# Performance work log

Hardware: AMD Instinct MI355X
Metric: run time of the kernel (lower is better)

## Reference

```python
import jax, jax.numpy as jnp
import numpy as np

B, S, D = 2, 2048, 1024
H, DH = 16, 64          # n_heads, size_per_head; H*DH == D
FF = 4096               # hidden_dim
EPS = 1e-6              # flax LayerNorm default


def _layernorm(x, scale, bias):
    mu = jnp.mean(x, axis=-1, keepdims=True)
    var = jnp.mean(jnp.square(x - mu), axis=-1, keepdims=True)
    return (x - mu) * jax.lax.rsqrt(var + EPS) * scale + bias


def setup_inputs() -> dict:
    key = jax.random.key(0)
    ks = jax.random.split(key, 12)
    p = lambda k, shape: (jax.random.normal(k, shape, dtype=jnp.float32) * 0.02)
    return {
        "X": jax.random.normal(ks[0], (B, S, D), dtype=jnp.float32),
        "mask": jax.random.randint(ks[1], (B, S), 0, 2, dtype=jnp.int32),
        "Wq": p(ks[2], (D, H * DH)), "bq": jnp.zeros((H * DH,), jnp.float32),
        "Wk": p(ks[3], (D, H * DH)), "bk": jnp.zeros((H * DH,), jnp.float32),
        "Wv": p(ks[4], (D, H * DH)), "bv": jnp.zeros((H * DH,), jnp.float32),
        "Wo": p(ks[5], (H * DH, D)), "bo": jnp.zeros((D,), jnp.float32),
        "ln0_scale": jnp.ones((D,), jnp.float32), "ln0_bias": jnp.zeros((D,), jnp.float32),
        "W1": p(ks[6], (D, FF)), "b1": jnp.zeros((FF,), jnp.float32),
        "W2": p(ks[7], (FF, D)), "b2": jnp.zeros((D,), jnp.float32),
        "ln1_scale": jnp.ones((D,), jnp.float32), "ln1_bias": jnp.zeros((D,), jnp.float32),
    }


def reference(X, mask, Wq, bq, Wk, bk, Wv, bv, Wo, bo,
              ln0_scale, ln0_bias, W1, b1, W2, b2, ln1_scale, ln1_bias):
    b, n, d = X.shape

    def proj(x, W, bias):
        # (B,S,D) -> (B,H,S,DH)
        return (x @ W + bias).reshape(b, n, H, DH).swapaxes(1, 2)

    q = proj(X, Wq, bq)
    k = proj(X, Wk, bk)
    v = proj(X, Wv, bv)

    # scaled dot-product attention with additive padding mask
    scores = jnp.einsum('bhnd,bhmd->bhnm', q, k) / jnp.sqrt(jnp.asarray(DH, X.dtype))
    m = mask[:, None, None, :].astype(scores.dtype)  # (B,1,1,M)
    scores = scores + m * -10000.0
    attn = jax.nn.softmax(scores, axis=-1)
    out = jnp.einsum('bhnm,bhmd->bhnd', attn, v)      # (B,H,S,DH)
    out = out.swapaxes(1, 2).reshape(b, n, H * DH)
    out = out @ Wo + bo

    # add & norm
    X1 = _layernorm(X + out, ln0_scale, ln0_bias)

    # feed-forward
    ff = jnp.maximum(X1 @ W1 + b1, 0.0) @ W2 + b2

    # add & norm
    return _layernorm(X1 + ff, ln1_scale, ln1_bias)
```

## Files before the change

### kernel.cpp

```cpp
#include <hip/hip_runtime.h>
#include <hip/hip_bf16.h>
#include <stdint.h>

#define B_ 2
#define S_ 2048
#define D_ 1024
#define H_ 16
#define DH_ 64
#define FF_ 4096
#define M_ (B_*S_)

typedef __bf16 bf16;
typedef __bf16 bf16x4 __attribute__((ext_vector_type(4)));
typedef __bf16 bf16x8 __attribute__((ext_vector_type(8)));
typedef float f32x4 __attribute__((ext_vector_type(4)));

#define LOG2E 1.44269504f

__device__ __forceinline__ float fexp2(float x) {
#if __has_builtin(__builtin_amdgcn_exp2f)
  return __builtin_amdgcn_exp2f(x);
#else
  return exp2f(x);
#endif
}

__device__ __forceinline__ void gload_lds16(const void* g, void* l) {
  auto gp = reinterpret_cast<const __attribute__((address_space(1))) void*>(
      reinterpret_cast<uintptr_t>(g));
  auto lp = reinterpret_cast<__attribute__((address_space(3))) void*>(
      reinterpret_cast<uintptr_t>(l));
  __builtin_amdgcn_global_load_lds(gp, lp, 16, 0, 0);
}

__global__ __launch_bounds__(256) void prep_all(
    const float* __restrict__ X, bf16* __restrict__ Xb,
    const float* __restrict__ bq, const float* __restrict__ bk,
    const float* __restrict__ bv, float* __restrict__ bqkv,
    const int* __restrict__ mask, float* __restrict__ Mp,
    const float* __restrict__ Wq, const float* __restrict__ Wk,
    const float* __restrict__ Wv, const float* __restrict__ Wo,
    const float* __restrict__ W1, const float* __restrict__ W2,
    bf16* __restrict__ Wqkvt, bf16* __restrict__ Wot,
    bf16* __restrict__ W1t, bf16* __restrict__ W2t) {
  int bid = blockIdx.x;
  const int tid = threadIdx.x;
  if (bid < 4096) {
    int i = (bid * 256 + tid) * 4;
    float4 v = *(const float4*)(X + i);
    Xb[i+0] = (bf16)v.x; Xb[i+1] = (bf16)v.y;
    Xb[i+2] = (bf16)v.z; Xb[i+3] = (bf16)v.w;
    return;
  }
  bid -= 4096;
  if (bid < 12) {
    int i = bid * 256 + tid;
    bqkv[i] = i < 1024 ? bq[i] : (i < 2048 ? bk[i-1024] : bv[i-2048]);
    return;
  }
  bid -= 12;
  if (bid < 16) {
    int i = bid * 256 + tid;
    Mp[i] = (-10000.0f * LOG2E) * (float)mask[i];
    return;
  }
  bid -= 16;
  const float* src; bf16* dst; int K, N;
  if (bid < 1024)      { src = Wq; dst = Wqkvt;                     K=1024; N=1024; }
  else if (bid < 2048) { src = Wk; dst = Wqkvt + (size_t)1024*1024; K=1024; N=1024; bid -= 1024; }
  else if (bid < 3072) { src = Wv; dst = Wqkvt + (size_t)2048*1024; K=1024; N=1024; bid -= 2048; }
  else if (bid < 4096) { src = Wo; dst = Wot;                       K=1024; N=1024; bid -= 3072; }
  else if (bid < 8192) { src = W1; dst = W1t;                       K=1024; N=4096; bid -= 4096; }
  else                 { src = W2; dst = W2t;                       K=4096; N=1024; bid -= 8192; }
  __shared__ float t[32][33];
  const int tx = tid & 31, ty = tid >> 5;
  const int nt32 = N >> 5;
  const int n0 = (bid % nt32) * 32, k0 = (bid / nt32) * 32;
#pragma unroll
  for (int i = 0; i < 4; i++)
    t[ty + i*8][tx] = src[(size_t)(k0 + ty + i*8) * N + n0 + tx];
  __syncthreads();
#pragma unroll
  for (int i = 0; i < 4; i++)
    dst[(size_t)(n0 + ty + i*8) * K + k0 + tx] = (bf16)t[tx][ty + i*8];
}
#define PREP_BLOCKS (4096 + 12 + 16 + 4*1024 + 2*4096)

__global__ __launch_bounds__(256) void transpose_v(
    const bf16* __restrict__ QKV, bf16* __restrict__ Vt) {
  __shared__ bf16 t[64][66];
  int bh = blockIdx.x, s0 = blockIdx.y * 64;
  int b = bh >> 4, h = bh & 15;
  int w = threadIdx.x >> 6, l = threadIdx.x & 63;
#pragma unroll
  for (int i = 0; i < 16; i++) {
    int sr = w*16 + i;
    t[sr][l] = QKV[(size_t)(b*S_ + s0 + sr) * 3072 + 2*D_ + h*DH_ + l];
  }
  __syncthreads();
  const int pcol = (l & 15) * 4 + (l >> 4);
#pragma unroll
  for (int i = 0; i < 16; i++) {
    int dh = w*16 + i;
    Vt[((size_t)(bh*DH_ + dh)) * S_ + s0 + pcol] = t[l][dh];
  }
}

template<int SK>
__global__ __launch_bounds__(256) void gemm_sk(
    const bf16* __restrict__ A, const bf16* __restrict__ Bt,
    const float* __restrict__ bias, float* __restrict__ Cp,
    int M, int N, int K) {
  __shared__ bf16 As[2][128*32];
  __shared__ bf16 Bs[2][128*32];
  const int tid = threadIdx.x;
  const int w = tid >> 6, l = tid & 63;
  const int wm = w >> 1, wn = w & 1;
  const int r16 = l & 15, g = l >> 4;

  const int gx = gridDim.x, gxy = gx * gridDim.y;
  const int nwg = gxy * SK;
  const int lid = (blockIdx.z * gridDim.y + blockIdx.y) * gx + blockIdx.x;
  const int swz = (lid & 7) * (nwg >> 3) + (lid >> 3);
  const int z = swz / gxy, rem = swz % gxy;
  const int m0 = (rem / gx) * 128, n0 = (rem % gx) * 128;
  const int kc = K / SK, kb = z * kc;

  const int srow = w*16 + (l >> 2);
  const int acol8 = (l & 3) * 8;
  const bf16* ag = A + (size_t)(m0 + srow) * K + acol8;
  const bf16* bg = Bt + (size_t)(n0 + srow) * K + acol8;

  f32x4 acc[4][4];
#pragma unroll
  for (int i = 0; i < 4; i++)
#pragma unroll
    for (int j = 0; j < 4; j++) acc[i][j] = (f32x4){0.f,0.f,0.f,0.f};

#pragma unroll
  for (int p = 0; p < 2; p++) {
    gload_lds16(ag + (size_t)(p*64) * K + kb, &As[0][(p*64 + w*16) * 32]);
    gload_lds16(bg + (size_t)(p*64) * K + kb, &Bs[0][(p*64 + w*16) * 32]);
  }
  asm volatile("s_waitcnt vmcnt(0)" ::: "memory");
  __builtin_amdgcn_s_barrier();
  asm volatile("" ::: "memory");

  const int nt = kc >> 5;
  int cur = 0;
  for (int t = 0; t < nt; ++t) {
    if (t + 1 < nt) {
      const int k0 = kb + (t + 1) * 32;
#pragma unroll
      for (int p = 0; p < 2; p++) {
        gload_lds16(ag + (size_t)(p*64) * K + k0, &As[cur^1][(p*64 + w*16) * 32]);
        gload_lds16(bg + (size_t)(p*64) * K + k0, &Bs[cur^1][(p*64 + w*16) * 32]);
      }
    }
    bf16x8 af[4], bfr[4];
#pragma unroll
    for (int mi = 0; mi < 4; mi++)
      af[mi] = *(const bf16x8*)&As[cur][(wm*64 + mi*16 + r16) * 32 + g*8];
#pragma unroll
    for (int ni = 0; ni < 4; ni++)
      bfr[ni] = *(const bf16x8*)&Bs[cur][(wn*64 + ni*16 + r16) * 32 + g*8];
    __builtin_amdgcn_s_setprio(1);
#pragma unroll
    for (int mi = 0; mi < 4; mi++)
#pragma unroll
      for (int ni = 0; ni < 4; ni++)
        acc[mi][ni] = __builtin_amdgcn_mfma_f32_16x16x32_bf16(
            af[mi], bfr[ni], acc[mi][ni], 0, 0, 0);
    __builtin_amdgcn_s_setprio(0);

    asm volatile("s_waitcnt vmcnt(0)" ::: "memory");
    __builtin_amdgcn_s_barrier();
    asm volatile("" ::: "memory");
    cur ^= 1;
  }

  float* outp = Cp + (size_t)z * M * N;
  float bvs[4];
#pragma unroll
  for (int ni = 0; ni < 4; ni++)
    bvs[ni] = (z == 0) ? bias[n0 + wn*64 + ni*16 + r16] : 0.f;
#pragma unroll
  for (int mi = 0; mi < 4; mi++)
#pragma unroll
    for (int ni = 0; ni < 4; ni++)
#pragma unroll
      for (int r = 0; r < 4; r++) {
        size_t row = (size_t)(m0 + wm*64 + mi*16 + g*4 + r);
        size_t col = (size_t)(n0 + wn*64 + ni*16 + r16);
        outp[row * N + col] = acc[mi][ni][r] + bvs[ni];
      }
}

template<bool RELU>
__global__ __launch_bounds__(512) void gemm256(
    const bf16* __restrict__ A, const bf16* __restrict__ Bt,
    const float* __restrict__ bias, bf16* __restrict__ C,
    int M, int N, int K) {
  __shared__ bf16 As[2][256*64];
  __shared__ bf16 Bs[2][256*64];
  const int tid = threadIdx.x;
  const int w = tid >> 6, l = tid & 63;
  const int wm = w >> 2, wn = w & 3;
  const int r16 = l & 15, g = l >> 4;

  const int gx = gridDim.x;
  const int nwg = gx * gridDim.y;
  const int lid = blockIdx.y * gx + blockIdx.x;
  const int swz = (lid & 7) * (nwg >> 3) + (lid >> 3);
  const int m0 = (swz / gx) * 256, n0 = (swz % gx) * 256;

  const int srow = w*8 + (l >> 3);
  const int sch  = ((l & 7) ^ (l >> 3)) * 8;
  const bf16* ag = A  + (size_t)(m0 + srow) * K + sch;
  const bf16* bg = Bt + (size_t)(n0 + srow) * K + sch;

  f32x4 acc[8][4];
#pragma unroll
  for (int i = 0; i < 8; i++)
#pragma unroll
    for (int j = 0; j < 4; j++) acc[i][j] = (f32x4){0.f,0.f,0.f,0.f};

#pragma unroll
  for (int q = 0; q < 4; q++) {
    gload_lds16(ag + (size_t)(q*64) * K, &As[0][(q*64 + w*8) * 64]);
    gload_lds16(bg + (size_t)(q*64) * K, &Bs[0][(q*64 + w*8) * 64]);
  }
  asm volatile("s_waitcnt vmcnt(0)" ::: "memory");
  __builtin_amdgcn_s_barrier();
  asm volatile("" ::: "memory");

  const int nt = K >> 6;
  int cur = 0;
  for (int t = 0; t < nt; ++t) {
    if (t + 1 < nt) {
      const size_t k0 = (size_t)(t + 1) << 6;
#pragma unroll
      for (int q = 0; q < 4; q++) {
        gload_lds16(ag + (size_t)(q*64) * K + k0, &As[cur^1][(q*64 + w*8) * 64]);
        gload_lds16(bg + (size_t)(q*64) * K + k0, &Bs[cur^1][(q*64 + w*8) * 64]);
      }
    }

    bf16x8 af[4][2], blo[2][2], bhi[2][2];
#pragma unroll
    for (int mi = 0; mi < 4; mi++)
#pragma unroll
      for (int kk = 0; kk < 2; kk++) {
        const int row = wm*128 + mi*16 + r16;
        af[mi][kk] = *(const bf16x8*)&As[cur][row*64 + (((kk*4+g) ^ (row & 7)))*8];
      }
#pragma unroll
    for (int ni = 0; ni < 2; ni++)
#pragma unroll
      for (int kk = 0; kk < 2; kk++) {
        const int row = wn*64 + ni*16 + r16;
        blo[ni][kk] = *(const bf16x8*)&Bs[cur][row*64 + (((kk*4+g) ^ (row & 7)))*8];
      }
    __builtin_amdgcn_s_setprio(1);
#pragma unroll
    for (int mi = 0; mi < 4; mi++)
#pragma unroll
      for (int ni = 0; ni < 2; ni++)
#pragma unroll
        for (int kk = 0; kk < 2; kk++)
          acc[mi][ni] = __builtin_amdgcn_mfma_f32_16x16x32_bf16(
              af[mi][kk], blo[ni][kk], acc[mi][ni], 0, 0, 0);
    __builtin_amdgcn_s_setprio(0);
#pragma unroll
    for (int ni = 0; ni < 2; ni++)
#pragma unroll
      for (int kk = 0; kk < 2; kk++) {
        const int row = wn*64 + 32 + ni*16 + r16;
        bhi[ni][kk] = *(const bf16x8*)&Bs[cur][row*64 + (((kk*4+g) ^ (row & 7)))*8];
      }
    __builtin_amdgcn_s_setprio(1);
#pragma unroll
    for (int mi = 0; mi < 4; mi++)
#pragma unroll
      for (int ni = 0; ni < 2; ni++)
#pragma unroll
        for (int kk = 0; kk < 2; kk++)
          acc[mi][2+ni] = __builtin_amdgcn_mfma_f32_16x16x32_bf16(
              af[mi][kk], bhi[ni][kk], acc[mi][2+ni], 0, 0, 0);
    __builtin_amdgcn_s_setprio(0);
#pragma unroll
    for (int mi = 0; mi < 4; mi++)
#pragma unroll
      for (int kk = 0; kk < 2; kk++) {
        const int row = wm*128 + 64 + mi*16 + r16;
        af[mi][kk] = *(const bf16x8*)&As[cur][row*64 + (((kk*4+g) ^ (row & 7)))*8];
      }
    __builtin_amdgcn_s_setprio(1);
#pragma unroll
    for (int mi = 0; mi < 4; mi++)
#pragma unroll
      for (int ni = 0; ni < 2; ni++)
#pragma unroll
        for (int kk = 0; kk < 2; kk++)
          acc[4+mi][2+ni] = __builtin_amdgcn_mfma_f32_16x16x32_bf16(
              af[mi][kk], bhi[ni][kk], acc[4+mi][2+ni], 0, 0, 0);
    __builtin_amdgcn_s_setprio(0);
    __builtin_amdgcn_s_setprio(1);
#pragma unroll
    for (int mi = 0; mi < 4; mi++)
#pragma unroll
      for (int ni = 0; ni < 2; ni++)
#pragma unroll
        for (int kk = 0; kk < 2; kk++)
          acc[4+mi][ni] = __builtin_amdgcn_mfma_f32_16x16x32_bf16(
              af[mi][kk], blo[ni][kk], acc[4+mi][ni], 0, 0, 0);
    __builtin_amdgcn_s_setprio(0);

    asm volatile("s_waitcnt vmcnt(0)" ::: "memory");
    __builtin_amdgcn_s_barrier();
    asm volatile("" ::: "memory");
    cur ^= 1;
  }

  float bvs[4];
#pragma unroll
  for (int ni = 0; ni < 4; ni++) bvs[ni] = bias[n0 + wn*64 + ni*16 + r16];
#pragma unroll
  for (int mi = 0; mi < 8; mi++)
#pragma unroll
    for (int ni = 0; ni < 4; ni++)
#pragma unroll
      for (int r = 0; r < 4; r++) {
        float v = acc[mi][ni][r] + bvs[ni];
        if (RELU) v = fmaxf(v, 0.f);
        C[(size_t)(m0 + wm*128 + mi*16 + g*4 + r) * N +
          (n0 + wn*64 + ni*16 + r16)] = (bf16)v;
      }
}

__global__ __launch_bounds__(256) void attn(
    const bf16* __restrict__ QKV, const bf16* __restrict__ Vt,
    const float* __restrict__ Mp, bf16* __restrict__ AO) {
  __shared__ bf16 Ks[2][64*64];
  __shared__ bf16 Vs[2][64*64];
  __shared__ bf16 Ps[4][32*72];

  const float SC2 = 0.125f * LOG2E;
  const int bh = blockIdx.x, b = bh >> 4, h = bh & 15;
  const int q0 = blockIdx.y * 128;
  const int tid = threadIdx.x, w = tid >> 6, l = tid & 63;
  const int r16 = l & 15, g = l >> 4;
  const int qw = q0 + w*32;

  bf16x8 qf[2][2];
#pragma unroll
  for (int s = 0; s < 2; s++)
#pragma unroll
    for (int kk = 0; kk < 2; kk++)
      qf[s][kk] = *(const bf16x8*)&QKV[((size_t)(b*S_ + qw + s*16 + r16))*3072
                                       + h*64 + kk*32 + g*8];

  const int srow = w*8 + (l >> 3);
  const int sch  = (l & 7) ^ (l >> 3);
  const bf16* kg = QKV + ((size_t)(b*S_) + srow)*3072 + 1024 + h*64 + sch*8;
  const bf16* vg = Vt + ((size_t)(bh*64 + srow))*S_ + sch*8;

  f32x4 po[2][4];
#pragma unroll
  for (int s = 0; s < 2; s++)
#pragma unroll
    for (int n = 0; n < 4; n++) po[s][n] = (f32x4){0.f,0.f,0.f,0.f};
  float mrun[8], lsum[8];
#pragma unroll
  for (int r = 0; r < 8; r++) { mrun[r] = -1.0e30f; lsum[r] = 0.f; }

  float madd[4];
#pragma unroll
  for (int ct = 0; ct < 4; ct++) madd[ct] = Mp[b*S_ + ct*16 + r16];
#pragma unroll
  for (int p = 0; p < 2; p++) {
    gload_lds16(kg + (size_t)(p*32)*3072, &Ks[0][(p*256 + w*64)*8]);
    gload_lds16(vg + (size_t)(p*32)*S_,   &Vs[0][(p*256 + w*64)*8]);
  }

  const int NT = S_/64;
  int cur = 0;
  for (int it = 0; it < NT; ++it) {
    const int kv0 = it * 64;
    if (it + 1 < NT) {
#pragma unroll
      for (int p = 0; p < 2; p++) {
        gload_lds16(kg + (size_t)(kv0 + 64 + p*32)*3072, &Ks[cur^1][(p*256 + w*64)*8]);
        gload_lds16(vg + (size_t)(p*32)*S_ + (kv0 + 64), &Vs[cur^1][(p*256 + w*64)*8]);
      }
      asm volatile("s_waitcnt vmcnt(4)" ::: "memory");
    } else {
      asm volatile("s_waitcnt vmcnt(0)" ::: "memory");
    }
    __builtin_amdgcn_s_barrier();
    asm volatile("" ::: "memory");

    float sv[2][4][4];
    __builtin_amdgcn_s_setprio(1);
#pragma unroll
    for (int ct = 0; ct < 4; ct++) {
      const int row = ct*16 + r16;
      bf16x8 kf0 = *(const bf16x8*)&Ks[cur][row*64 + ((g) ^ (row & 7))*8];
      bf16x8 kf1 = *(const bf16x8*)&Ks[cur][row*64 + ((4+g) ^ (row & 7))*8];
      f32x4 a0 = (f32x4){0.f,0.f,0.f,0.f}, a1 = (f32x4){0.f,0.f,0.f,0.f};
      a0 = __builtin_amdgcn_mfma_f32_16x16x32_bf16(qf[0][0], kf0, a0, 0, 0, 0);
      a0 = __builtin_amdgcn_mfma_f32_16x16x32_bf16(qf[0][1], kf1, a0, 0, 0, 0);
      a1 = __builtin_amdgcn_mfma_f32_16x16x32_bf16(qf[1][0], kf0, a1, 0, 0, 0);
      a1 = __builtin_amdgcn_mfma_f32_16x16x32_bf16(qf[1][1], kf1, a1, 0, 0, 0);
#pragma unroll
      for (int r = 0; r < 4; r++) {
        sv[0][ct][r] = a0[r]*SC2 + madd[ct];
        sv[1][ct][r] = a1[r]*SC2 + madd[ct];
      }
    }
    __builtin_amdgcn_s_setprio(0);

    if (it + 1 < NT) {
#pragma unroll
      for (int ct = 0; ct < 4; ct++)
        madd[ct] = Mp[b*S_ + kv0 + 64 + ct*16 + r16];
    }

    float lmax[8];
#pragma unroll
    for (int s = 0; s < 2; s++)
#pragma unroll
      for (int r = 0; r < 4; r++)
        lmax[s*4+r] = fmaxf(fmaxf(sv[s][0][r], sv[s][1][r]),
                            fmaxf(sv[s][2][r], sv[s][3][r]));
    bool grow = false;
#pragma unroll
    for (int i = 0; i < 8; i++) grow |= (lmax[i] > mrun[i] + 8.f);
    if (__any(grow)) {
#pragma unroll
      for (int s = 0; s < 2; s++)
#pragma unroll
        for (int r = 0; r < 4; r++) {
          const int i = s*4 + r;
          float t = lmax[i];
#pragma unroll
          for (int off = 8; off >= 1; off >>= 1) t = fmaxf(t, __shfl_xor(t, off, 16));
          float mnew = fmaxf(mrun[i], t);
          float sc = fexp2(mrun[i] - mnew);
          mrun[i] = mnew;
          lsum[i] *= sc;
#pragma unroll
          for (int n = 0; n < 4; n++) po[s][n][r] *= sc;
        }
    }
#pragma unroll
    for (int s = 0; s < 2; s++)
#pragma unroll
      for (int r = 0; r < 4; r++) {
        const int i = s*4 + r;
#pragma unroll
        for (int ct = 0; ct < 4; ct++)
          sv[s][ct][r] = fexp2(sv[s][ct][r] - mrun[i]);
        lsum[i] += (sv[s][0][r] + sv[s][1][r]) + (sv[s][2][r] + sv[s][3][r]);
      }

#pragma unroll
    for (int s = 0; s < 2; s++)
#pragma unroll
      for (int r = 0; r < 4; r++) {
        bf16x4 pk;
#pragma unroll
        for (int ct = 0; ct < 4; ct++) pk[ct] = (bf16)sv[s][ct][r];
        *(bf16x4*)&Ps[w][(s*16 + g*4 + r)*72 + r16*4] = pk;
      }
    asm volatile("s_waitcnt lgkmcnt(0)" ::: "memory");

    __builtin_amdgcn_s_setprio(1);
#pragma unroll
    for (int kk = 0; kk < 2; kk++) {
      bf16x8 pa0 = *(const bf16x8*)&Ps[w][(r16)*72 + kk*32 + g*8];
      bf16x8 pa1 = *(const bf16x8*)&Ps[w][(16 + r16)*72 + kk*32 + g*8];
#pragma unroll
      for (int n = 0; n < 4; n++) {
        const int row = n*16 + r16;
        bf16x8 vf = *(const bf16x8*)&Vs[cur][row*64 + ((kk*4 + g) ^ (row & 7))*8];
        po[0][n] = __builtin_amdgcn_mfma_f32_16x16x32_bf16(pa0, vf, po[0][n], 0, 0, 0);
        po[1][n] = __builtin_amdgcn_mfma_f32_16x16x32_bf16(pa1, vf, po[1][n], 0, 0, 0);
      }
    }
    __builtin_amdgcn_s_setprio(0);

    __builtin_amdgcn_s_barrier();
    asm volatile("" ::: "memory");
    cur ^= 1;
  }

#pragma unroll
  for (int i = 0; i < 8; i++) {
    float t = lsum[i];
#pragma unroll
    for (int off = 8; off >= 1; off >>= 1) t += __shfl_xor(t, off, 16);
    lsum[i] = t;
  }

#pragma unroll
  for (int s = 0; s < 2; s++)
#pragma unroll
    for (int n = 0; n < 4; n++)
#pragma unroll
      for (int r = 0; r < 4; r++) {
        float v = po[s][n][r] / lsum[s*4 + r];
        AO[(size_t)(b*S_ + qw + s*16 + g*4 + r)*D_ + h*64 + n*16 + r16] = (bf16)v;
      }
}

template<bool XF32, bool OUTF32>
__global__ __launch_bounds__(256) void ln_res2(
    const void* __restrict__ xp, const float* __restrict__ p0,
    const float* __restrict__ p1, const float* __restrict__ sc,
    const float* __restrict__ bi, float* __restrict__ y,
    bf16* __restrict__ yb) {
  const int row = blockIdx.x, tid = threadIdx.x;
  const size_t base = (size_t)row * D_;
  float xv[4];
  if (XF32) {
    float4 a = ((const float4*)((const float*)xp + base))[tid];
    xv[0] = a.x; xv[1] = a.y; xv[2] = a.z; xv[3] = a.w;
  } else {
    bf16x4 a = ((const bf16x4*)((const bf16*)xp + base))[tid];
#pragma unroll
    for (int j = 0; j < 4; j++) xv[j] = (float)a[j];
  }
  float4 a0 = ((const float4*)(p0 + base))[tid];
  float4 a1 = ((const float4*)(p1 + base))[tid];
  float v[4] = {xv[0] + a0.x + a1.x, xv[1] + a0.y + a1.y,
                xv[2] + a0.z + a1.z, xv[3] + a0.w + a1.w};
  float s  = v[0] + v[1] + v[2] + v[3];
  float ss = v[0]*v[0] + v[1]*v[1] + v[2]*v[2] + v[3]*v[3];
#pragma unroll
  for (int off = 32; off >= 1; off >>= 1) {
    s  += __shfl_xor(s, off, 64);
    ss += __shfl_xor(ss, off, 64);
  }
  __shared__ float red[8];
  const int wv = tid >> 6;
  if ((tid & 63) == 0) { red[wv] = s; red[4 + wv] = ss; }
  __syncthreads();
  s  = red[0] + red[1] + red[2] + red[3];
  ss = red[4] + red[5] + red[6] + red[7];
  const float mu  = s * (1.0f / D_);
  const float inv = rsqrtf(ss * (1.0f / D_) - mu*mu + 1e-6f);
  float4 scv = ((const float4*)sc)[tid];
  float4 biv = ((const float4*)bi)[tid];
  float o[4];
  o[0] = (v[0]-mu)*inv*scv.x + biv.x;
  o[1] = (v[1]-mu)*inv*scv.y + biv.y;
  o[2] = (v[2]-mu)*inv*scv.z + biv.z;
  o[3] = (v[3]-mu)*inv*scv.w + biv.w;
  if (OUTF32) {
    ((float4*)(y + base))[tid] = make_float4(o[0], o[1], o[2], o[3]);
  } else {
    bf16x4 ob;
#pragma unroll
    for (int j = 0; j < 4; j++) ob[j] = (bf16)o[j];
    *(bf16x4*)&yb[base + tid*4] = ob;
  }
}

extern "C" void kernel_launch(void* const* d_in, const int* in_sizes, int n_in,
                              void* d_out, int out_size, void* d_ws, size_t ws_size,
                              hipStream_t stream) {
  const float* X    = (const float*)d_in[0];
  const int*   mask = (const int*)d_in[1];
  const float* Wq   = (const float*)d_in[2];
  const float* bq   = (const float*)d_in[3];
  const float* Wk   = (const float*)d_in[4];
  const float* bk   = (const float*)d_in[5];
  const float* Wv   = (const float*)d_in[6];
  const float* bv   = (const float*)d_in[7];
  const float* Wo   = (const float*)d_in[8];
  const float* bo   = (const float*)d_in[9];
  const float* ln0s = (const float*)d_in[10];
  const float* ln0b = (const float*)d_in[11];
  const float* W1   = (const float*)d_in[12];
  const float* b1   = (const float*)d_in[13];
  const float* W2   = (const float*)d_in[14];
  const float* b2   = (const float*)d_in[15];
  const float* ln1s = (const float*)d_in[16];
  const float* ln1b = (const float*)d_in[17];
  float* out = (float*)d_out;

  char* ws = (char*)d_ws;
  const size_t MB = 1024 * 1024;
  bf16*  Xb    = (bf16*)(ws + 0);
  bf16*  AO    = (bf16*)(ws + 0);
  bf16*  X1b   = (bf16*)(ws + 0);
  bf16*  Wqkvt = (bf16*)(ws + 8*MB);
  bf16*  Wot   = (bf16*)(ws + 14*MB);
  bf16*  W1t   = (bf16*)(ws + 16*MB);
  bf16*  W2t   = (bf16*)(ws + 24*MB);
  bf16*  QKV   = (bf16*)(ws + 32*MB);
  bf16*  Vt    = (bf16*)(ws + 56*MB);
  bf16*  FF1   = (bf16*)(ws + 32*MB);
  float* P0    = (float*)(ws + 64*MB);
  float* P1    = (float*)(ws + 80*MB);
  float* bqkv  = (float*)(ws + 64*MB);
  float* Mp    = (float*)(ws + 64*MB + 16384);

  prep_all<<<PREP_BLOCKS, 256, 0, stream>>>(
      X, Xb, bq, bk, bv, bqkv, mask, Mp,
      Wq, Wk, Wv, Wo, W1, W2, Wqkvt, Wot, W1t, W2t);

  gemm256<false><<<dim3(3072/256, M_/256), 512, 0, stream>>>(Xb, Wqkvt, bqkv, QKV, M_, 3072, D_);
  transpose_v<<<dim3(32, S_/64), 256, 0, stream>>>(QKV, Vt);
  attn<<<dim3(32, S_/128), 256, 0, stream>>>(QKV, Vt, Mp, AO);
  gemm_sk<2><<<dim3(D_/128, M_/128, 2), 256, 0, stream>>>(AO, Wot, bo, P0, M_, D_, D_);
  ln_res2<true,false><<<M_, 256, 0, stream>>>(X, P0, P1, ln0s, ln0b, nullptr, X1b);
  gemm256<true><<<dim3(FF_/256, M_/256), 512, 0, stream>>>(X1b, W1t, b1, FF1, M_, FF_, D_);
  gemm_sk<2><<<dim3(D_/128, M_/128, 2), 256, 0, stream>>>(FF1, W2t, b2, P0, M_, D_, FF_);
  ln_res2<false,true><<<M_, 256, 0, stream>>>(X1b, P0, P1, ln1s, ln1b, out, nullptr);
}
```

Measured before the change: 228.0 us.

## Split attention over two KV halves with a combine kernel

The attention kernel now splits the key/value sequence into two halves along a new grid dimension, doubling the block count from 512 to 1024. Each half writes unnormalized bf16 partial outputs plus per-row max and sum, and a new attn_combine kernel merges them with log-sum-exp rescaling. The P tile in shared memory shrinks to one 16-row subtile processed per s iteration with swizzled addressing, and launch bounds request 4 blocks per CU to raise occupancy. In exchange it adds an extra launch, extra global traffic for the partials, and bf16 rounding of unnormalized partial outputs.

```diff
diff --git a/kernel.cpp b/kernel.cpp
--- a/kernel.cpp
+++ b/kernel.cpp
@@ -338,16 +338,19 @@
       }
 }
 
-__global__ __launch_bounds__(256) void attn(
+__global__ __launch_bounds__(256, 4) void attn(
     const bf16* __restrict__ QKV, const bf16* __restrict__ Vt,
-    const float* __restrict__ Mp, bf16* __restrict__ AO) {
+    const float* __restrict__ Mp, bf16* __restrict__ Op,
+    float2* __restrict__ ML) {
   __shared__ bf16 Ks[2][64*64];
   __shared__ bf16 Vs[2][64*64];
-  __shared__ bf16 Ps[4][32*72];
+  __shared__ bf16 Ps[4][16*64];
 
   const float SC2 = 0.125f * LOG2E;
   const int bh = blockIdx.x, b = bh >> 4, h = bh & 15;
   const int q0 = blockIdx.y * 128;
+  const int z  = blockIdx.z;
+  const int kvb = z * (S_/2);
   const int tid = threadIdx.x, w = tid >> 6, l = tid & 63;
   const int r16 = l & 15, g = l >> 4;
   const int qw = q0 + w*32;
@@ -362,8 +365,8 @@
 
   const int srow = w*8 + (l >> 3);
   const int sch  = (l & 7) ^ (l >> 3);
-  const bf16* kg = QKV + ((size_t)(b*S_) + srow)*3072 + 1024 + h*64 + sch*8;
-  const bf16* vg = Vt + ((size_t)(bh*64 + srow))*S_ + sch*8;
+  const bf16* kg = QKV + ((size_t)(b*S_) + kvb + srow)*3072 + 1024 + h*64 + sch*8;
+  const bf16* vg = Vt + ((size_t)(bh*64 + srow))*S_ + kvb + sch*8;
 
   f32x4 po[2][4];
 #pragma unroll
@@ -376,14 +379,14 @@
 
   float madd[4];
 #pragma unroll
-  for (int ct = 0; ct < 4; ct++) madd[ct] = Mp[b*S_ + ct*16 + r16];
+  for (int ct = 0; ct < 4; ct++) madd[ct] = Mp[b*S_ + kvb + ct*16 + r16];
 #pragma unroll
   for (int p = 0; p < 2; p++) {
     gload_lds16(kg + (size_t)(p*32)*3072, &Ks[0][(p*256 + w*64)*8]);
     gload_lds16(vg + (size_t)(p*32)*S_,   &Vs[0][(p*256 + w*64)*8]);
   }
 
-  const int NT = S_/64;
+  const int NT = (S_/2)/64;
   int cur = 0;
   for (int it = 0; it < NT; ++it) {
     const int kv0 = it * 64;
@@ -423,7 +426,7 @@
     if (it + 1 < NT) {
 #pragma unroll
       for (int ct = 0; ct < 4; ct++)
-        madd[ct] = Mp[b*S_ + kv0 + 64 + ct*16 + r16];
+        madd[ct] = Mp[b*S_ + kvb + kv0 + 64 + ct*16 + r16];
     }
 
     float lmax[8];
@@ -465,30 +468,30 @@
       }
 
 #pragma unroll
-    for (int s = 0; s < 2; s++)
+    for (int s = 0; s < 2; s++) {
 #pragma unroll
       for (int r = 0; r < 4; r++) {
         bf16x4 pk;
 #pragma unroll
         for (int ct = 0; ct < 4; ct++) pk[ct] = (bf16)sv[s][ct][r];
-        *(bf16x4*)&Ps[w][(s*16 + g*4 + r)*72 + r16*4] = pk;
-      }
-    asm volatile("s_waitcnt lgkmcnt(0)" ::: "memory");
-
-    __builtin_amdgcn_s_setprio(1);
-#pragma unroll
-    for (int kk = 0; kk < 2; kk++) {
-      bf16x8 pa0 = *(const bf16x8*)&Ps[w][(r16)*72 + kk*32 + g*8];
-      bf16x8 pa1 = *(const bf16x8*)&Ps[w][(16 + r16)*72 + kk*32 + g*8];
-#pragma unroll
-      for (int n = 0; n < 4; n++) {
-        const int row = n*16 + r16;
-        bf16x8 vf = *(const bf16x8*)&Vs[cur][row*64 + ((kk*4 + g) ^ (row & 7))*8];
-        po[0][n] = __builtin_amdgcn_mfma_f32_16x16x32_bf16(pa0, vf, po[0][n], 0, 0, 0);
-        po[1][n] = __builtin_amdgcn_mfma_f32_16x16x32_bf16(pa1, vf, po[1][n], 0, 0, 0);
-      }
+        const int row = g*4 + r;
+        const int c = (r16 >> 1) ^ (row & 7);
+        *(bf16x4*)&Ps[w][row*64 + c*8 + (r16 & 1)*4] = pk;
+      }
+      asm volatile("s_waitcnt lgkmcnt(0)" ::: "memory");
+      __builtin_amdgcn_s_setprio(1);
+#pragma unroll
+      for (int kk = 0; kk < 2; kk++) {
+        bf16x8 pa = *(const bf16x8*)&Ps[w][r16*64 + (((kk*4+g) ^ (r16 & 7)))*8];
+#pragma unroll
+        for (int n = 0; n < 4; n++) {
+          const int row = n*16 + r16;
+          bf16x8 vf = *(const bf16x8*)&Vs[cur][row*64 + ((kk*4 + g) ^ (row & 7))*8];
+          po[s][n] = __builtin_amdgcn_mfma_f32_16x16x32_bf16(pa, vf, po[s][n], 0, 0, 0);
+        }
+      }
+      __builtin_amdgcn_s_setprio(0);
     }
-    __builtin_amdgcn_s_setprio(0);
 
     __builtin_amdgcn_s_barrier();
     asm volatile("" ::: "memory");
@@ -508,10 +511,40 @@
 #pragma unroll
     for (int n = 0; n < 4; n++)
 #pragma unroll
-      for (int r = 0; r < 4; r++) {
-        float v = po[s][n][r] / lsum[s*4 + r];
-        AO[(size_t)(b*S_ + qw + s*16 + g*4 + r)*D_ + h*64 + n*16 + r16] = (bf16)v;
-      }
+      for (int r = 0; r < 4; r++)
+        Op[(size_t)z*M_*D_ + (size_t)(b*S_ + qw + s*16 + g*4 + r)*D_
+           + h*64 + n*16 + r16] = (bf16)po[s][n][r];
+  if (r16 == 0) {
+#pragma unroll
+    for (int s = 0; s < 2; s++)
+#pragma unroll
+      for (int r = 0; r < 4; r++)
+        ML[((size_t)z*32 + bh)*S_ + qw + s*16 + g*4 + r] =
+            make_float2(mrun[s*4 + r], lsum[s*4 + r]);
+  }
+}
+
+__global__ __launch_bounds__(256) void attn_combine(
+    const bf16* __restrict__ Op, const float2* __restrict__ ML,
+    bf16* __restrict__ AO) {
+  const int t = blockIdx.x;
+  const int tid = threadIdx.x;
+  const int d0 = tid * 4;
+  const int h = d0 >> 6;
+  const int q = t & (S_ - 1), b = t >> 11;
+  const int bh = b*16 + h;
+  float2 ml0 = ML[(size_t)bh*S_ + q];
+  float2 ml1 = ML[((size_t)32 + bh)*S_ + q];
+  float m = fmaxf(ml0.x, ml1.x);
+  float a0 = fexp2(ml0.x - m), a1 = fexp2(ml1.x - m);
+  float inv = 1.0f / (ml0.y*a0 + ml1.y*a1);
+  bf16x4 o0 = *(const bf16x4*)&Op[(size_t)t*D_ + d0];
+  bf16x4 o1 = *(const bf16x4*)&Op[(size_t)M_*D_ + (size_t)t*D_ + d0];
+  bf16x4 o;
+#pragma unroll
+  for (int j = 0; j < 4; j++)
+    o[j] = (bf16)(((float)o0[j]*a0 + (float)o1[j]*a1) * inv);
+  *(bf16x4*)&AO[(size_t)t*D_ + d0] = o;
 }
 
 template<bool XF32, bool OUTF32>
@@ -527,7 +560,7 @@
     float4 a = ((const float4*)((const float*)xp + base))[tid];
     xv[0] = a.x; xv[1] = a.y; xv[2] = a.z; xv[3] = a.w;
   } else {
-    bf16x4 a = ((const bf16x4*)((const bf16*)xp + base))[tid];
+    bf16x4 a = *(const bf16x4*)&((const bf16*)xp)[base + tid*4];
 #pragma unroll
     for (int j = 0; j < 4; j++) xv[j] = (float)a[j];
   }
@@ -592,20 +625,22 @@
 
   char* ws = (char*)d_ws;
   const size_t MB = 1024 * 1024;
-  bf16*  Xb    = (bf16*)(ws + 0);
-  bf16*  AO    = (bf16*)(ws + 0);
-  bf16*  X1b   = (bf16*)(ws + 0);
-  bf16*  Wqkvt = (bf16*)(ws + 8*MB);
-  bf16*  Wot   = (bf16*)(ws + 14*MB);
-  bf16*  W1t   = (bf16*)(ws + 16*MB);
-  bf16*  W2t   = (bf16*)(ws + 24*MB);
-  bf16*  QKV   = (bf16*)(ws + 32*MB);
-  bf16*  Vt    = (bf16*)(ws + 56*MB);
-  bf16*  FF1   = (bf16*)(ws + 32*MB);
-  float* P0    = (float*)(ws + 64*MB);
-  float* P1    = (float*)(ws + 80*MB);
-  float* bqkv  = (float*)(ws + 64*MB);
-  float* Mp    = (float*)(ws + 64*MB + 16384);
+  bf16*   Xb    = (bf16*)(ws + 0);
+  bf16*   AO    = (bf16*)(ws + 0);
+  bf16*   X1b   = (bf16*)(ws + 0);
+  bf16*   Wqkvt = (bf16*)(ws + 8*MB);
+  bf16*   Wot   = (bf16*)(ws + 14*MB);
+  bf16*   W1t   = (bf16*)(ws + 16*MB);
+  bf16*   W2t   = (bf16*)(ws + 24*MB);
+  bf16*   QKV   = (bf16*)(ws + 32*MB);
+  bf16*   Vt    = (bf16*)(ws + 56*MB);
+  bf16*   FF1   = (bf16*)(ws + 32*MB);
+  bf16*   Op    = (bf16*)(ws + 64*MB);
+  float*  P0    = (float*)(ws + 64*MB);
+  float*  P1    = (float*)(ws + 80*MB);
+  float*  bqkv  = (float*)(ws + 80*MB);
+  float*  Mp    = (float*)(ws + 80*MB + 16384);
+  float2* ML    = (float2*)(ws + 90*MB);
 
   prep_all<<<PREP_BLOCKS, 256, 0, stream>>>(
       X, Xb, bq, bk, bv, bqkv, mask, Mp,
@@ -613,7 +648,8 @@
 
   gemm256<false><<<dim3(3072/256, M_/256), 512, 0, stream>>>(Xb, Wqkvt, bqkv, QKV, M_, 3072, D_);
   transpose_v<<<dim3(32, S_/64), 256, 0, stream>>>(QKV, Vt);
-  attn<<<dim3(32, S_/128), 256, 0, stream>>>(QKV, Vt, Mp, AO);
+  attn<<<dim3(32, S_/128, 2), 256, 0, stream>>>(QKV, Vt, Mp, Op, ML);
+  attn_combine<<<M_, 256, 0, stream>>>(Op, ML, AO);
   gemm_sk<2><<<dim3(D_/128, M_/128, 2), 256, 0, stream>>>(AO, Wot, bo, P0, M_, D_, D_);
   ln_res2<true,false><<<M_, 256, 0, stream>>>(X, P0, P1, ln0s, ln0b, nullptr, X1b);
   gemm256<true><<<dim3(FF_/256, M_/256), 512, 0, stream>>>(X1b, W1t, b1, FF1, M_, FF_, D_);
```

Result: slower. 258.0 us (+13.1%).

## Double GEMM K-tile to 64 with XOR-swizzled LDS layout

Applied to the files above, without the earlier changes.

The split-K GEMM now stages 64-wide K tiles instead of 32, so each barrier and wait covers twice as many MFMAs and the number of loop iterations halves. The LDS rows are XOR-swizzled on 16-byte chunks, both when loading from global memory and when reading fragments, to avoid bank conflicts on the wider rows. The cost is double the LDS footprint (64KB per block), which may lower occupancy. A bf16 load in the layernorm is rewritten with equivalent addressing.

```diff
diff --git a/kernel.cpp b/kernel.cpp
--- a/kernel.cpp
+++ b/kernel.cpp
@@ -111,8 +111,8 @@
     const bf16* __restrict__ A, const bf16* __restrict__ Bt,
     const float* __restrict__ bias, float* __restrict__ Cp,
     int M, int N, int K) {
-  __shared__ bf16 As[2][128*32];
-  __shared__ bf16 Bs[2][128*32];
+  __shared__ bf16 As[2][128*64];
+  __shared__ bf16 Bs[2][128*64];
   const int tid = threadIdx.x;
   const int w = tid >> 6, l = tid & 63;
   const int wm = w >> 1, wn = w & 1;
@@ -126,10 +126,10 @@
   const int m0 = (rem / gx) * 128, n0 = (rem % gx) * 128;
   const int kc = K / SK, kb = z * kc;
 
-  const int srow = w*16 + (l >> 2);
-  const int acol8 = (l & 3) * 8;
-  const bf16* ag = A + (size_t)(m0 + srow) * K + acol8;
-  const bf16* bg = Bt + (size_t)(n0 + srow) * K + acol8;
+  const int srow = w*8 + (l >> 3);
+  const int sch  = ((l & 7) ^ (l >> 3)) * 8;
+  const bf16* ag = A + (size_t)(m0 + srow) * K + sch;
+  const bf16* bg = Bt + (size_t)(n0 + srow) * K + sch;
 
   f32x4 acc[4][4];
 #pragma unroll
@@ -138,39 +138,49 @@
     for (int j = 0; j < 4; j++) acc[i][j] = (f32x4){0.f,0.f,0.f,0.f};
 
 #pragma unroll
-  for (int p = 0; p < 2; p++) {
-    gload_lds16(ag + (size_t)(p*64) * K + kb, &As[0][(p*64 + w*16) * 32]);
-    gload_lds16(bg + (size_t)(p*64) * K + kb, &Bs[0][(p*64 + w*16) * 32]);
+  for (int q = 0; q < 4; q++) {
+    gload_lds16(ag + (size_t)(q*32) * K + kb, &As[0][(q*32 + w*8) * 64]);
+    gload_lds16(bg + (size_t)(q*32) * K + kb, &Bs[0][(q*32 + w*8) * 64]);
   }
   asm volatile("s_waitcnt vmcnt(0)" ::: "memory");
   __builtin_amdgcn_s_barrier();
   asm volatile("" ::: "memory");
 
-  const int nt = kc >> 5;
+  const int nt = kc >> 6;
   int cur = 0;
   for (int t = 0; t < nt; ++t) {
     if (t + 1 < nt) {
-      const int k0 = kb + (t + 1) * 32;
-#pragma unroll
-      for (int p = 0; p < 2; p++) {
-        gload_lds16(ag + (size_t)(p*64) * K + k0, &As[cur^1][(p*64 + w*16) * 32]);
-        gload_lds16(bg + (size_t)(p*64) * K + k0, &Bs[cur^1][(p*64 + w*16) * 32]);
+      const int k0 = kb + (t + 1) * 64;
+#pragma unroll
+      for (int q = 0; q < 4; q++) {
+        gload_lds16(ag + (size_t)(q*32) * K + k0, &As[cur^1][(q*32 + w*8) * 64]);
+        gload_lds16(bg + (size_t)(q*32) * K + k0, &Bs[cur^1][(q*32 + w*8) * 64]);
       }
     }
-    bf16x8 af[4], bfr[4];
-#pragma unroll
-    for (int mi = 0; mi < 4; mi++)
-      af[mi] = *(const bf16x8*)&As[cur][(wm*64 + mi*16 + r16) * 32 + g*8];
+    bf16x8 af[4][2], bfr[4][2];
+#pragma unroll
+    for (int mi = 0; mi < 4; mi++)
+#pragma unroll
+      for (int kk = 0; kk < 2; kk++) {
+        const int row = wm*64 + mi*16 + r16;
+        af[mi][kk] = *(const bf16x8*)&As[cur][row*64 + (((kk*4+g) ^ (row & 7)))*8];
+      }
 #pragma unroll
     for (int ni = 0; ni < 4; ni++)
-      bfr[ni] = *(const bf16x8*)&Bs[cur][(wn*64 + ni*16 + r16) * 32 + g*8];
+#pragma unroll
+      for (int kk = 0; kk < 2; kk++) {
+        const int row = wn*64 + ni*16 + r16;
+        bfr[ni][kk] = *(const bf16x8*)&Bs[cur][row*64 + (((kk*4+g) ^ (row & 7)))*8];
+      }
     __builtin_amdgcn_s_setprio(1);
 #pragma unroll
     for (int mi = 0; mi < 4; mi++)
 #pragma unroll
       for (int ni = 0; ni < 4; ni++)
-        acc[mi][ni] = __builtin_amdgcn_mfma_f32_16x16x32_bf16(
-            af[mi], bfr[ni], acc[mi][ni], 0, 0, 0);
+#pragma unroll
+        for (int kk = 0; kk < 2; kk++)
+          acc[mi][ni] = __builtin_amdgcn_mfma_f32_16x16x32_bf16(
+              af[mi][kk], bfr[ni][kk], acc[mi][ni], 0, 0, 0);
     __builtin_amdgcn_s_setprio(0);
 
     asm volatile("s_waitcnt vmcnt(0)" ::: "memory");
@@ -527,7 +537,7 @@
     float4 a = ((const float4*)((const float*)xp + base))[tid];
     xv[0] = a.x; xv[1] = a.y; xv[2] = a.z; xv[3] = a.w;
   } else {
-    bf16x4 a = ((const bf16x4*)((const bf16*)xp + base))[tid];
+    bf16x4 a = *(const bf16x4*)&((const bf16*)xp)[base + tid*4];
 #pragma unroll
     for (int j = 0; j < 4; j++) xv[j] = (float)a[j];
   }
```

New measurement: 228.3 us. No clear change (+0.1%).
